# Optimization experiments

Hardware: AMD Instinct MI355X
Metric: run time of the kernel (lower is better)

Reference implementation:

```python
import jax, jax.numpy as jnp
import numpy as np

B, T, D = 2, 2048, 1024
H = 16
HD = D // H          # 64
WIN = 512            # sliding window size


def _band_mask(t, win):
    i = jnp.arange(t)[:, None]
    j = jnp.arange(t)[None, :]
    return ((j <= i) & (j > i - win)).astype(jnp.float32)


def setup_inputs() -> dict:
    key = jax.random.key(0)
    ks = jax.random.split(key, 7)
    s = 0.02
    return {
        "x":  jax.random.normal(ks[0], (B, T, D), dtype=jnp.float32),
        "Wg": jax.random.normal(ks[1], (D, D), dtype=jnp.float32) * s,
        "bg": jnp.zeros((D,), dtype=jnp.float32),
        "Wv": jax.random.normal(ks[2], (D, H * HD), dtype=jnp.float32) * s,
        "bv": jnp.zeros((H * HD,), dtype=jnp.float32),
        "Wo": jax.random.normal(ks[3], (D, D), dtype=jnp.float32) * s,
        "bo": jnp.zeros((D,), dtype=jnp.float32),
    }


def genetic_fitness(pop, mask):
    # pop: (B,H,T,D_head); mask: (T,T)
    # gene_means[b,h,i,d] = sum_j mask[i,j]*pop[b,h,j,d] / active_counts[i]
    counts = jnp.maximum(mask.sum(axis=1), 1.0)                 # (T,)
    gene_means = jnp.einsum('ij,bhjd->bhid', mask, pop) / counts[None, None, :, None]
    denom = gene_means + 0.5                                    # (B,H,T,Dh)
    sum_inv = (1.0 / denom).sum(axis=-1, keepdims=True)
    gene_fit = 1.0 / (denom * sum_inv)                          # (B,H,T,Dh)
    # org_fitness[b,h,i,j] = mask[i,j] * <gene_fit[b,h,i], pop[b,h,j]>
    org = mask[None, None] * jnp.einsum('bhid,bhjd->bhij', gene_fit, pop)
    row = jnp.maximum(org.sum(axis=-1, keepdims=True), 1e-10)
    return org / row                                            # (B,H,T,T)


def reference(x, Wg, bg, Wv, bv, Wo, bo):
    mask = _band_mask(T, WIN)
    g = (x @ Wg + bg).reshape(B, T, H, HD).transpose(0, 2, 1, 3)   # (B,H,T,Dh)
    v = (x @ Wv + bv).reshape(B, T, H, HD).transpose(0, 2, 1, 3)   # (B,H,T,Dh)
    attn = genetic_fitness(g, mask)                                 # (B,H,T,T)
    out = jnp.einsum('bhij,bhjd->bhid', attn, v)                    # (B,H,T,Dh)
    out = out.transpose(0, 2, 1, 3).reshape(B, T, D)
    return out @ Wo + bo
```

## Files before the change

### kernel.cpp

```cpp
#include <hip/hip_runtime.h>

#define NB 2
#define NT 2048
#define ND 1024
#define NH 16
#define HD 64
#define WIN 512
#define NBH (NB*NH)
#define NCH (NT/64)

typedef short    bf16x8 __attribute__((ext_vector_type(8)));
typedef unsigned short us8 __attribute__((ext_vector_type(8)));
typedef unsigned short us4 __attribute__((ext_vector_type(4)));
typedef float    f32x4  __attribute__((ext_vector_type(4)));

__device__ __forceinline__ void fma16(const float4 av, const float4 bv, float acc[4][4])
{
    float ar[4] = {av.x, av.y, av.z, av.w};
    float br[4] = {bv.x, bv.y, bv.z, bv.w};
#pragma unroll
    for (int r = 0; r < 4; ++r)
#pragma unroll
        for (int c = 0; c < 4; ++c)
            acc[r][c] = fmaf(ar[r], br[c], acc[r][c]);
}

__device__ __forceinline__ void split_bf16(float f, unsigned short& h, unsigned short& l)
{
    unsigned u = __float_as_uint(f);
    h = (unsigned short)(u >> 16);
    float fh = __uint_as_float(u & 0xffff0000u);
    l = (unsigned short)(__float_as_uint(f - fh) >> 16);
}

__device__ __forceinline__ unsigned short bf_rne(float f)
{
    unsigned u = __float_as_uint(f);
    u += 0x7fffu + ((u >> 16) & 1u);
    return (unsigned short)(u >> 16);
}

__device__ __forceinline__ us8 pack8(float4 a, float4 b)
{
    us8 r;
    r[0] = bf_rne(a.x); r[1] = bf_rne(a.y); r[2] = bf_rne(a.z); r[3] = bf_rne(a.w);
    r[4] = bf_rne(b.x); r[5] = bf_rne(b.y); r[6] = bf_rne(b.z); r[7] = bf_rne(b.w);
    return r;
}

__global__ __launch_bounds__(256)
void gemm_k(const float* __restrict__ A, const float* __restrict__ W,
            const float* __restrict__ bias, float* __restrict__ C,
            int M, int N, int K)
{
    __shared__ float As[16][64];
    __shared__ float Bs[16][64];
    const int tid = threadIdx.x;
    const int tx = tid & 15, ty = tid >> 4;
    const int n0 = blockIdx.x << 6, m0 = blockIdx.y << 6;
    const int am = tid >> 2, ak = (tid & 3) << 2;
    const int bk = tid >> 4, bn = (tid & 15) << 2;
    const float* Ap = A + (size_t)(m0 + am) * K + ak;
    const float* Wp = W + (size_t)bk * N + n0 + bn;

    float4 a4 = *(const float4*)(Ap);
    float4 b4 = *(const float4*)(Wp);
    float acc[4][4] = {};
    for (int k0 = 0; k0 < K; k0 += 16) {
        __syncthreads();
        {
            const int sw = (tid & 3) << 4;
            As[ak + 0][am ^ sw] = a4.x;
            As[ak + 1][am ^ sw] = a4.y;
            As[ak + 2][am ^ sw] = a4.z;
            As[ak + 3][am ^ sw] = a4.w;
            *(float4*)&Bs[bk][bn] = b4;
        }
        __syncthreads();
        if (k0 + 16 < K) {
            a4 = *(const float4*)(Ap + k0 + 16);
            b4 = *(const float4*)(Wp + (size_t)(k0 + 16) * N);
        }
#pragma unroll
        for (int k = 0; k < 16; ++k) {
            const float4 av = *(const float4*)&As[k][(ty << 2) ^ ((k & 12) << 2)];
            const float4 bv = *(const float4*)&Bs[k][tx << 2];
            fma16(av, bv, acc);
        }
    }
    const float4 bias4 = *(const float4*)&bias[n0 + (tx << 2)];
    const float bb[4] = {bias4.x, bias4.y, bias4.z, bias4.w};
#pragma unroll
    for (int r = 0; r < 4; ++r) {
        const int row = m0 + (ty << 2) + r;
        float4 o;
        o.x = acc[r][0] + bb[0]; o.y = acc[r][1] + bb[1];
        o.z = acc[r][2] + bb[2]; o.w = acc[r][3] + bb[3];
        const int b = row >> 11;
        const int i = row & (NT - 1);
        const int h = n0 >> 6;
        *(float4*)&C[((((size_t)(b * NH + h)) << 11) + i) * HD + (tx << 2)] = o;
    }
}

template<int MODE>
__global__ __launch_bounds__(256)
void mgemm_k(const unsigned short* __restrict__ Ahi, const unsigned short* __restrict__ Alo,
             const unsigned short* __restrict__ Bhi, const unsigned short* __restrict__ Blo,
             const float* __restrict__ bias, float* __restrict__ C,
             int M, int N, int K)
{
    __shared__ unsigned short As[2][128 * 32];
    __shared__ unsigned short Bs[2][128 * 32];
    const int tid = threadIdx.x;
    const int wave = tid >> 6, lane = tid & 63;
    const int wm = wave >> 1, wn = wave & 1;
    const int m0 = blockIdx.y << 7, n0 = blockIdx.x << 7;

    const int srow = tid >> 1, skh = tid & 1;
    const int ssw = (srow & 3) ^ ((srow >> 2) & 3);
    const int sA0 = srow * 32 + ((((skh << 1) | 0) ^ ssw) << 3);
    const int sA1 = srow * 32 + ((((skh << 1) | 1) ^ ssw) << 3);
    const size_t aoff = (size_t)(m0 + srow) * K + (skh << 4);
    const size_t boff = (size_t)(n0 + srow) * K + (skh << 4);

    us8 ah0 = *(const us8*)(Ahi + aoff), ah1 = *(const us8*)(Ahi + aoff + 8);
    us8 al0 = *(const us8*)(Alo + aoff), al1 = *(const us8*)(Alo + aoff + 8);
    us8 bh0 = *(const us8*)(Bhi + boff), bh1 = *(const us8*)(Bhi + boff + 8);
    us8 bl0 = *(const us8*)(Blo + boff), bl1 = *(const us8*)(Blo + boff + 8);

    const int fsw = ((lane >> 4) ^ (lane & 3) ^ ((lane & 12) >> 2)) << 3;

    f32x4 acc[4][4] = {};
    for (int k0 = 0; k0 < K; k0 += 32) {
        __syncthreads();
        *(us8*)&As[0][sA0] = ah0; *(us8*)&As[0][sA1] = ah1;
        *(us8*)&As[1][sA0] = al0; *(us8*)&As[1][sA1] = al1;
        *(us8*)&Bs[0][sA0] = bh0; *(us8*)&Bs[0][sA1] = bh1;
        *(us8*)&Bs[1][sA0] = bl0; *(us8*)&Bs[1][sA1] = bl1;
        __syncthreads();
        if (k0 + 32 < K) {
            const size_t ka = aoff + k0 + 32, kb = boff + k0 + 32;
            ah0 = *(const us8*)(Ahi + ka); ah1 = *(const us8*)(Ahi + ka + 8);
            al0 = *(const us8*)(Alo + ka); al1 = *(const us8*)(Alo + ka + 8);
            bh0 = *(const us8*)(Bhi + kb); bh1 = *(const us8*)(Bhi + kb + 8);
            bl0 = *(const us8*)(Blo + kb); bl1 = *(const us8*)(Blo + kb + 8);
        }
        bf16x8 aH[4], aL[4], bH[4], bL[4];
#pragma unroll
        for (int s = 0; s < 4; ++s) {
            const int ra = (wm << 6) + (s << 4) + (lane & 15);
            const int rb = (wn << 6) + (s << 4) + (lane & 15);
            aH[s] = *(const bf16x8*)&As[0][ra * 32 + fsw];
            aL[s] = *(const bf16x8*)&As[1][ra * 32 + fsw];
            bH[s] = *(const bf16x8*)&Bs[0][rb * 32 + fsw];
            bL[s] = *(const bf16x8*)&Bs[1][rb * 32 + fsw];
        }
#pragma unroll
        for (int ms = 0; ms < 4; ++ms)
#pragma unroll
            for (int ns = 0; ns < 4; ++ns) {
                acc[ms][ns] = __builtin_amdgcn_mfma_f32_16x16x32_bf16(aH[ms], bH[ns], acc[ms][ns], 0, 0, 0);
                acc[ms][ns] = __builtin_amdgcn_mfma_f32_16x16x32_bf16(aH[ms], bL[ns], acc[ms][ns], 0, 0, 0);
                acc[ms][ns] = __builtin_amdgcn_mfma_f32_16x16x32_bf16(aL[ms], bH[ns], acc[ms][ns], 0, 0, 0);
            }
    }

#pragma unroll
    for (int ms = 0; ms < 4; ++ms)
#pragma unroll
        for (int ns = 0; ns < 4; ++ns) {
            const int col = n0 + (wn << 6) + (ns << 4) + (lane & 15);
            const float bb = bias[col];
#pragma unroll
            for (int r = 0; r < 4; ++r) {
                const int row = m0 + (wm << 6) + (ms << 4) + ((lane >> 4) << 2) + r;
                const float val = acc[ms][ns][r] + bb;
                if (MODE == 0) {
                    C[(size_t)row * N + col] = val;
                } else {
                    const int b = row >> 11, i = row & (NT - 1);
                    const int h = col >> 6;
                    C[((((size_t)(b * NH + h)) << 11) + i) * HD + (col & 63)] = val;
                }
            }
        }
}

__global__ __launch_bounds__(256)
void split_k(const float* __restrict__ x, unsigned short* __restrict__ xh,
             unsigned short* __restrict__ xl)
{
    const int e0 = (blockIdx.x * 256 + threadIdx.x) << 2;
    const float4 v = *(const float4*)&x[e0];
    ushort4 hh, ll;
    split_bf16(v.x, hh.x, ll.x); split_bf16(v.y, hh.y, ll.y);
    split_bf16(v.z, hh.z, ll.z); split_bf16(v.w, hh.w, ll.w);
    *(ushort4*)&xh[e0] = hh;
    *(ushort4*)&xl[e0] = ll;
}

__global__ __launch_bounds__(256)
void tsplit_k(const float* __restrict__ W, unsigned short* __restrict__ Th,
              unsigned short* __restrict__ Tl)
{
    __shared__ float Ls[64][68];
    const int n0 = blockIdx.x << 6, k0 = blockIdx.y << 6;
    const int tid = threadIdx.x;
    const int r16 = tid >> 4, c4 = (tid & 15) << 2;
#pragma unroll
    for (int j = 0; j < 4; ++j) {
        const int row = r16 + (j << 4);
        *(float4*)&Ls[row][c4] = *(const float4*)&W[(size_t)(k0 + row) * ND + n0 + c4];
    }
    __syncthreads();
#pragma unroll
    for (int j = 0; j < 4; ++j) {
        const int n = r16 + (j << 4);
        ushort4 hh, ll;
        split_bf16(Ls[c4 + 0][n], hh.x, ll.x);
        split_bf16(Ls[c4 + 1][n], hh.y, ll.y);
        split_bf16(Ls[c4 + 2][n], hh.z, ll.z);
        split_bf16(Ls[c4 + 3][n], hh.w, ll.w);
        const size_t o = (size_t)(n0 + n) * ND + k0 + c4;
        *(ushort4*)&Th[o] = hh;
        *(ushort4*)&Tl[o] = ll;
    }
}

__global__ __launch_bounds__(64)
void chunkscan_k(const float* __restrict__ g, float* __restrict__ Pin,
                 float* __restrict__ Csum)
{
    const int blk = blockIdx.x;
    const int lane = threadIdx.x;
    const int base = (blk << 12) + lane;
    float run = 0.f;
#pragma unroll 16
    for (int t = 0; t < 64; ++t) {
        run += g[base + (t << 6)];
        Pin[base + (t << 6)] = run;
    }
    Csum[(blk << 6) + lane] = run;
}

__global__ __launch_bounds__(64)
void chunkpre_k(const float* __restrict__ Csum, float* __restrict__ Cpre)
{
    const int bh = blockIdx.x, lane = threadIdx.x;
    float run = 0.f;
    for (int c = 0; c < NCH; ++c) {
        run += Csum[((bh * NCH + c) << 6) + lane];
        Cpre[((bh * NCH + c) << 6) + lane] = run;
    }
}

__global__ __launch_bounds__(256)
void winsum_k(const float* __restrict__ Pin, const float* __restrict__ Cpre,
              float* __restrict__ wout)
{
    const int idx = blockIdx.x * 256 + threadIdx.x;
    const int e0 = idx << 2;
    const int row = e0 >> 6;
    const int d = e0 & 63;
    const int bh = row >> 11;
    const int i = row & (NT - 1);
    const int c = i >> 6;

    float4 p = *(const float4*)&Pin[e0];
    float ax = p.x, ay = p.y, az = p.z, aw = p.w;
    if (c > 0) {
        const float4 q = *(const float4*)&Cpre[((bh * NCH + c - 1) << 6) + d];
        ax += q.x; ay += q.y; az += q.z; aw += q.w;
    }
    if (i >= WIN) {
        const int i2 = i - WIN;
        const int c2 = i2 >> 6;
        const float4 p2 = *(const float4*)&Pin[(((bh << 11) + i2) << 6) + d];
        ax -= p2.x; ay -= p2.y; az -= p2.z; aw -= p2.w;
        if (c2 > 0) {
            const float4 q2 = *(const float4*)&Cpre[((bh * NCH + c2 - 1) << 6) + d];
            ax -= q2.x; ay -= q2.y; az -= q2.z; aw -= q2.w;
        }
    }
    *(float4*)&wout[e0] = make_float4(ax, ay, az, aw);
}

__global__ __launch_bounds__(256)
void stats_k(float* __restrict__ wing, double* __restrict__ rowsum)
{
    const int row = (blockIdx.x << 2) + (threadIdx.x >> 6);
    const int lane = threadIdx.x & 63;
    const int i = row & (NT - 1);
    const float w = wing[(row << 6) + lane];
    const double cnt = (double)((i + 1 < WIN) ? (i + 1) : WIN);
    const double denom = (double)w / cnt + 0.5;
    double s = 1.0 / denom;
#pragma unroll
    for (int off = 32; off > 0; off >>= 1) s += __shfl_xor(s, off);
    const double gf = 1.0 / (denom * s);
    double rw = gf * (double)w;
#pragma unroll
    for (int off = 32; off > 0; off >>= 1) rw += __shfl_xor(rw, off);
    wing[(row << 6) + lane] = (float)gf;
    if (lane == 0) rowsum[row] = rw;
}

__global__ __launch_bounds__(256)
void attn_k(const float* __restrict__ gf, const float* __restrict__ g,
            const float* __restrict__ v, const double* __restrict__ rowsum,
            unsigned short* __restrict__ aoh, unsigned short* __restrict__ aol)
{
    __shared__ unsigned short gL[64 * 72];
    __shared__ unsigned short VT[64 * 72];
    __shared__ unsigned short SL[64 * 72];

    const int bh = blockIdx.y, it = blockIdx.x;
    const int i0 = it << 6;
    const int tid = threadIdx.x;
    const int wave = tid >> 6, lane = tid & 63;
    const int l15 = lane & 15, l4 = lane >> 4;

    bf16x8 gfB[2];
    {
        const int ig = i0 + (wave << 4) + l15;
        const float* src = gf + (((size_t)(bh << 11) + ig) << 6) + (l4 << 3);
        const float4 q0 = *(const float4*)(src);
        const float4 q1 = *(const float4*)(src + 4);
        const float4 q2 = *(const float4*)(src + 32);
        const float4 q3 = *(const float4*)(src + 36);
        const us8 f0 = pack8(q0, q1), f1 = pack8(q2, q3);
        gfB[0] = (bf16x8)f0;
        gfB[1] = (bf16x8)f1;
    }

    const int sj = lane, sd0 = wave << 4;

    const int t_lo = (it >= 8) ? (it - 8) : 0;
    float4 gq[4], vq[4];
    {
        const float* gsrc = g + (((size_t)(bh << 11) + (t_lo << 6) + sj) << 6) + sd0;
        const float* vsrc = v + (((size_t)(bh << 11) + (t_lo << 6) + sj) << 6) + sd0;
#pragma unroll
        for (int q = 0; q < 4; ++q) gq[q] = *(const float4*)(gsrc + (q << 2));
#pragma unroll
        for (int q = 0; q < 4; ++q) vq[q] = *(const float4*)(vsrc + (q << 2));
    }

    f32x4 acc2[4] = {};
    const int ig_mask = i0 + (wave << 4) + l15;

    for (int t = t_lo; t <= it; ++t) {
        const int j0 = t << 6;
        __syncthreads();
        {
            *(us8*)&gL[sj * 72 + sd0]     = pack8(gq[0], gq[1]);
            *(us8*)&gL[sj * 72 + sd0 + 8] = pack8(gq[2], gq[3]);
            const float* vf = (const float*)vq;
#pragma unroll
            for (int h = 0; h < 16; ++h)
                VT[(sd0 + h) * 72 + sj] = bf_rne(vf[h]);
        }
        __syncthreads();

        if (t < it) {
            const float* gsrc = g + (((size_t)(bh << 11) + j0 + 64 + sj) << 6) + sd0;
            const float* vsrc = v + (((size_t)(bh << 11) + j0 + 64 + sj) << 6) + sd0;
#pragma unroll
            for (int q = 0; q < 4; ++q) gq[q] = *(const float4*)(gsrc + (q << 2));
#pragma unroll
            for (int q = 0; q < 4; ++q) vq[q] = *(const float4*)(vsrc + (q << 2));
        }

        f32x4 sfr[4] = {};
#pragma unroll
        for (int kk = 0; kk < 2; ++kk)
#pragma unroll
            for (int jm = 0; jm < 4; ++jm) {
                const bf16x8 ag = *(const bf16x8*)&gL[((jm << 4) + l15) * 72 + (kk << 5) + (l4 << 3)];
                sfr[jm] = __builtin_amdgcn_mfma_f32_16x16x32_bf16(ag, gfB[kk], sfr[jm], 0, 0, 0);
            }

        const bool need_mask = (t == it) || (t == it - 8);
#pragma unroll
        for (int jm = 0; jm < 4; ++jm) {
            float s0 = sfr[jm][0], s1 = sfr[jm][1], s2 = sfr[jm][2], s3 = sfr[jm][3];
            if (need_mask) {
                const int jb = j0 + (jm << 4) + (l4 << 2);
                if (!(jb + 0 <= ig_mask && jb + 0 > ig_mask - WIN)) s0 = 0.f;
                if (!(jb + 1 <= ig_mask && jb + 1 > ig_mask - WIN)) s1 = 0.f;
                if (!(jb + 2 <= ig_mask && jb + 2 > ig_mask - WIN)) s2 = 0.f;
                if (!(jb + 3 <= ig_mask && jb + 3 > ig_mask - WIN)) s3 = 0.f;
            }
            us4 sl;
            sl[0] = bf_rne(s0); sl[1] = bf_rne(s1); sl[2] = bf_rne(s2); sl[3] = bf_rne(s3);
            *(us4*)&SL[((wave << 4) + l15) * 72 + (jm << 4) + (l4 << 2)] = sl;
        }

#pragma unroll
        for (int kk = 0; kk < 2; ++kk) {
            const bf16x8 a2 = *(const bf16x8*)&SL[((wave << 4) + l15) * 72 + (kk << 5) + (l4 << 3)];
#pragma unroll
            for (int nf = 0; nf < 4; ++nf) {
                const bf16x8 b2 = *(const bf16x8*)&VT[((nf << 4) + l15) * 72 + (kk << 5) + (l4 << 3)];
                acc2[nf] = __builtin_amdgcn_mfma_f32_16x16x32_bf16(a2, b2, acc2[nf], 0, 0, 0);
            }
        }
    }

    const int b = bh >> 4, hh = bh & 15;
    float inv[4];
#pragma unroll
    for (int r = 0; r < 4; ++r) {
        const int ig = i0 + (wave << 4) + (l4 << 2) + r;
        double rs = rowsum[(bh << 11) + ig];
        if (!(rs > 1e-10)) rs = 1e-10;
        inv[r] = (float)(1.0 / rs);
    }
#pragma unroll
    for (int nf = 0; nf < 4; ++nf)
#pragma unroll
        for (int r = 0; r < 4; ++r) {
            const int ig = i0 + (wave << 4) + (l4 << 2) + r;
            const int d = (nf << 4) + l15;
            const float val = acc2[nf][r] * inv[r];
            unsigned short vh, vl;
            split_bf16(val, vh, vl);
            const size_t base = (((size_t)(b * NT + ig)) << 10) + (hh << 6) + d;
            aoh[base] = vh;
            aol[base] = vl;
        }
}

extern "C" void kernel_launch(void* const* d_in, const int* in_sizes, int n_in,
                              void* d_out, int out_size, void* d_ws, size_t ws_size,
                              hipStream_t stream)
{
    const float* x  = (const float*)d_in[0];
    const float* Wg = (const float*)d_in[1];
    const float* bg = (const float*)d_in[2];
    const float* Wv = (const float*)d_in[3];
    const float* bv = (const float*)d_in[4];
    const float* Wo = (const float*)d_in[5];
    const float* bo = (const float*)d_in[6];
    float* out = (float*)d_out;

    const size_t SZ = (size_t)NB * NH * NT * HD;
    const size_t MW = (size_t)ND * ND;
    const size_t CS = (size_t)NBH * NCH * HD;

    float* gbuf = (float*)d_ws;
    float* vbuf = gbuf + SZ;
    float* pinb = vbuf + SZ;
    float* winb = pinb + SZ;
    float* wpl  = winb + SZ;
    float* csum = wpl + 2 * MW;
    float* cpre = csum + CS;
    double* rsum = (double*)(cpre + CS);

    unsigned short* xhi  = (unsigned short*)winb;
    unsigned short* xlo  = xhi + SZ;
    unsigned short* wvTh = (unsigned short*)wpl;
    unsigned short* wvTl = wvTh + MW;
    unsigned short* woTh = wvTl + MW;
    unsigned short* woTl = woTh + MW;
    unsigned short* aoh  = (unsigned short*)pinb;
    unsigned short* aol  = aoh + SZ;

    const int M = NB * NT;

    gemm_k<<<dim3(ND >> 6, M >> 6), 256, 0, stream>>>(x, Wg, bg, gbuf, M, ND, ND);
    split_k<<<(int)(SZ / 4 / 256), 256, 0, stream>>>(x, xhi, xlo);
    tsplit_k<<<dim3(ND >> 6, ND >> 6), 256, 0, stream>>>(Wv, wvTh, wvTl);
    tsplit_k<<<dim3(ND >> 6, ND >> 6), 256, 0, stream>>>(Wo, woTh, woTl);
    mgemm_k<1><<<dim3(ND >> 7, M >> 7), 256, 0, stream>>>(xhi, xlo, wvTh, wvTl, bv, vbuf, M, ND, ND);
    chunkscan_k<<<NBH * NCH, 64, 0, stream>>>(gbuf, pinb, csum);
    chunkpre_k<<<NBH, 64, 0, stream>>>(csum, cpre);
    winsum_k<<<(NBH * NT * HD / 4) / 256, 256, 0, stream>>>(pinb, cpre, winb);
    stats_k<<<(NBH * NT) / 4, 256, 0, stream>>>(winb, rsum);
    attn_k<<<dim3(NT >> 6, NBH), 256, 0, stream>>>(winb, gbuf, vbuf, rsum, aoh, aol);
    mgemm_k<0><<<dim3(ND >> 7, M >> 7), 256, 0, stream>>>(aoh, aol, woTh, woTl, bo, out, M, ND, ND);
}
```

Before: 388.7 us.

## Compute g projection with three-way bf16-split MFMA GEMM instead of FP32 SIMT

The FP32 SIMT GEMM for the g projection is replaced by a matrix-core GEMM. Both x and Wg are split into three bf16 parts, and six cross products are accumulated to keep near-FP32 accuracy. The goal is to move the largest projection from vector ALUs to MFMA units. The cost is extra split and transpose-split kernels, more workspace, and six times the MFMA work. The split of x now uses round-to-nearest for its high and middle parts, and these are also reused for the v projection.

```diff
diff --git a/kernel.cpp b/kernel.cpp
--- a/kernel.cpp
+++ b/kernel.cpp
@@ -14,17 +14,6 @@
 typedef unsigned short us4 __attribute__((ext_vector_type(4)));
 typedef float    f32x4  __attribute__((ext_vector_type(4)));
 
-__device__ __forceinline__ void fma16(const float4 av, const float4 bv, float acc[4][4])
-{
-    float ar[4] = {av.x, av.y, av.z, av.w};
-    float br[4] = {bv.x, bv.y, bv.z, bv.w};
-#pragma unroll
-    for (int r = 0; r < 4; ++r)
-#pragma unroll
-        for (int c = 0; c < 4; ++c)
-            acc[r][c] = fmaf(ar[r], br[c], acc[r][c]);
-}
-
 __device__ __forceinline__ void split_bf16(float f, unsigned short& h, unsigned short& l)
 {
     unsigned u = __float_as_uint(f);
@@ -40,6 +29,18 @@
     return (unsigned short)(u >> 16);
 }
 
+__device__ __forceinline__ void split3(float f, unsigned short& h,
+                                       unsigned short& m, unsigned short& l)
+{
+    h = bf_rne(f);
+    const float fh = __uint_as_float((unsigned)h << 16);
+    const float r1 = f - fh;
+    m = bf_rne(r1);
+    const float fm = __uint_as_float((unsigned)m << 16);
+    const float r2 = r1 - fm;
+    l = bf_rne(r2);
+}
+
 __device__ __forceinline__ us8 pack8(float4 a, float4 b)
 {
     us8 r;
@@ -49,58 +50,97 @@
 }
 
 __global__ __launch_bounds__(256)
-void gemm_k(const float* __restrict__ A, const float* __restrict__ W,
-            const float* __restrict__ bias, float* __restrict__ C,
-            int M, int N, int K)
-{
-    __shared__ float As[16][64];
-    __shared__ float Bs[16][64];
+void mgemm3_k(const unsigned short* __restrict__ Ah, const unsigned short* __restrict__ Am,
+              const unsigned short* __restrict__ Al,
+              const unsigned short* __restrict__ Bh, const unsigned short* __restrict__ Bm,
+              const unsigned short* __restrict__ Bl,
+              const float* __restrict__ bias, float* __restrict__ C,
+              int M, int N, int K)
+{
+    __shared__ unsigned short As[3][128 * 32];
+    __shared__ unsigned short Bs[3][128 * 32];
     const int tid = threadIdx.x;
-    const int tx = tid & 15, ty = tid >> 4;
-    const int n0 = blockIdx.x << 6, m0 = blockIdx.y << 6;
-    const int am = tid >> 2, ak = (tid & 3) << 2;
-    const int bk = tid >> 4, bn = (tid & 15) << 2;
-    const float* Ap = A + (size_t)(m0 + am) * K + ak;
-    const float* Wp = W + (size_t)bk * N + n0 + bn;
-
-    float4 a4 = *(const float4*)(Ap);
-    float4 b4 = *(const float4*)(Wp);
-    float acc[4][4] = {};
-    for (int k0 = 0; k0 < K; k0 += 16) {
+    const int wave = tid >> 6, lane = tid & 63;
+    const int wm = wave >> 1, wn = wave & 1;
+    const int m0 = blockIdx.y << 7, n0 = blockIdx.x << 7;
+    const int l15 = lane & 15;
+
+    const int srow = tid >> 1, skh = tid & 1;
+    const int ssw = (srow & 3) ^ ((srow >> 2) & 3);
+    const int sA0 = srow * 32 + ((((skh << 1) | 0) ^ ssw) << 3);
+    const int sA1 = srow * 32 + ((((skh << 1) | 1) ^ ssw) << 3);
+    const size_t aoff = (size_t)(m0 + srow) * K + (skh << 4);
+    const size_t boff = (size_t)(n0 + srow) * K + (skh << 4);
+
+    us8 a0[2], a1[2], a2[2], b0[2], b1[2], b2[2];
+    a0[0] = *(const us8*)(Ah + aoff); a0[1] = *(const us8*)(Ah + aoff + 8);
+    a1[0] = *(const us8*)(Am + aoff); a1[1] = *(const us8*)(Am + aoff + 8);
+    a2[0] = *(const us8*)(Al + aoff); a2[1] = *(const us8*)(Al + aoff + 8);
+    b0[0] = *(const us8*)(Bh + boff); b0[1] = *(const us8*)(Bh + boff + 8);
+    b1[0] = *(const us8*)(Bm + boff); b1[1] = *(const us8*)(Bm + boff + 8);
+    b2[0] = *(const us8*)(Bl + boff); b2[1] = *(const us8*)(Bl + boff + 8);
+
+    const int fsw = ((lane >> 4) ^ (lane & 3) ^ ((lane & 12) >> 2)) << 3;
+
+    f32x4 acc[4][4] = {};
+    for (int k0 = 0; k0 < K; k0 += 32) {
         __syncthreads();
-        {
-            const int sw = (tid & 3) << 4;
-            As[ak + 0][am ^ sw] = a4.x;
-            As[ak + 1][am ^ sw] = a4.y;
-            As[ak + 2][am ^ sw] = a4.z;
-            As[ak + 3][am ^ sw] = a4.w;
-            *(float4*)&Bs[bk][bn] = b4;
-        }
+        *(us8*)&As[0][sA0] = a0[0]; *(us8*)&As[0][sA1] = a0[1];
+        *(us8*)&As[1][sA0] = a1[0]; *(us8*)&As[1][sA1] = a1[1];
+        *(us8*)&As[2][sA0] = a2[0]; *(us8*)&As[2][sA1] = a2[1];
+        *(us8*)&Bs[0][sA0] = b0[0]; *(us8*)&Bs[0][sA1] = b0[1];
+        *(us8*)&Bs[1][sA0] = b1[0]; *(us8*)&Bs[1][sA1] = b1[1];
+        *(us8*)&Bs[2][sA0] = b2[0]; *(us8*)&Bs[2][sA1] = b2[1];
         __syncthreads();
-        if (k0 + 16 < K) {
-            a4 = *(const float4*)(Ap + k0 + 16);
-            b4 = *(const float4*)(Wp + (size_t)(k0 + 16) * N);
-        }
-#pragma unroll
-        for (int k = 0; k < 16; ++k) {
-            const float4 av = *(const float4*)&As[k][(ty << 2) ^ ((k & 12) << 2)];
-            const float4 bv = *(const float4*)&Bs[k][tx << 2];
-            fma16(av, bv, acc);
-        }
-    }
-    const float4 bias4 = *(const float4*)&bias[n0 + (tx << 2)];
-    const float bb[4] = {bias4.x, bias4.y, bias4.z, bias4.w};
-#pragma unroll
-    for (int r = 0; r < 4; ++r) {
-        const int row = m0 + (ty << 2) + r;
-        float4 o;
-        o.x = acc[r][0] + bb[0]; o.y = acc[r][1] + bb[1];
-        o.z = acc[r][2] + bb[2]; o.w = acc[r][3] + bb[3];
-        const int b = row >> 11;
-        const int i = row & (NT - 1);
-        const int h = n0 >> 6;
-        *(float4*)&C[((((size_t)(b * NH + h)) << 11) + i) * HD + (tx << 2)] = o;
-    }
+        if (k0 + 32 < K) {
+            const size_t ka = aoff + k0 + 32, kb = boff + k0 + 32;
+            a0[0] = *(const us8*)(Ah + ka); a0[1] = *(const us8*)(Ah + ka + 8);
+            a1[0] = *(const us8*)(Am + ka); a1[1] = *(const us8*)(Am + ka + 8);
+            a2[0] = *(const us8*)(Al + ka); a2[1] = *(const us8*)(Al + ka + 8);
+            b0[0] = *(const us8*)(Bh + kb); b0[1] = *(const us8*)(Bh + kb + 8);
+            b1[0] = *(const us8*)(Bm + kb); b1[1] = *(const us8*)(Bm + kb + 8);
+            b2[0] = *(const us8*)(Bl + kb); b2[1] = *(const us8*)(Bl + kb + 8);
+        }
+        bf16x8 aF[3][4], bF[3][4];
+#pragma unroll
+        for (int s = 0; s < 4; ++s) {
+            const int ra = (wm << 6) + (s << 4) + l15;
+            const int rb = (wn << 6) + (s << 4) + l15;
+#pragma unroll
+            for (int p = 0; p < 3; ++p) {
+                aF[p][s] = *(const bf16x8*)&As[p][ra * 32 + fsw];
+                bF[p][s] = *(const bf16x8*)&Bs[p][rb * 32 + fsw];
+            }
+        }
+#pragma unroll
+        for (int ms = 0; ms < 4; ++ms)
+#pragma unroll
+            for (int ns = 0; ns < 4; ++ns) {
+                f32x4 t = acc[ms][ns];
+                t = __builtin_amdgcn_mfma_f32_16x16x32_bf16(aF[0][ms], bF[0][ns], t, 0, 0, 0);
+                t = __builtin_amdgcn_mfma_f32_16x16x32_bf16(aF[0][ms], bF[1][ns], t, 0, 0, 0);
+                t = __builtin_amdgcn_mfma_f32_16x16x32_bf16(aF[1][ms], bF[0][ns], t, 0, 0, 0);
+                t = __builtin_amdgcn_mfma_f32_16x16x32_bf16(aF[0][ms], bF[2][ns], t, 0, 0, 0);
+                t = __builtin_amdgcn_mfma_f32_16x16x32_bf16(aF[2][ms], bF[0][ns], t, 0, 0, 0);
+                t = __builtin_amdgcn_mfma_f32_16x16x32_bf16(aF[1][ms], bF[1][ns], t, 0, 0, 0);
+                acc[ms][ns] = t;
+            }
+    }
+
+#pragma unroll
+    for (int ms = 0; ms < 4; ++ms)
+#pragma unroll
+        for (int ns = 0; ns < 4; ++ns) {
+            const int col = n0 + (wn << 6) + (ns << 4) + l15;
+            const float bb = bias[col];
+            const int h = col >> 6, d = col & 63;
+#pragma unroll
+            for (int r = 0; r < 4; ++r) {
+                const int row = m0 + (wm << 6) + (ms << 4) + ((lane >> 4) << 2) + r;
+                const int b = row >> 11, i = row & (NT - 1);
+                C[((((size_t)(b * NH + h)) << 11) + i) * HD + d] = acc[ms][ns][r] + bb;
+            }
+        }
 }
 
 template<int MODE>
@@ -188,15 +228,16 @@
 }
 
 __global__ __launch_bounds__(256)
-void split_k(const float* __restrict__ x, unsigned short* __restrict__ xh,
-             unsigned short* __restrict__ xl)
+void split3_k(const float* __restrict__ x, unsigned short* __restrict__ xh,
+              unsigned short* __restrict__ xm, unsigned short* __restrict__ xl)
 {
     const int e0 = (blockIdx.x * 256 + threadIdx.x) << 2;
     const float4 v = *(const float4*)&x[e0];
-    ushort4 hh, ll;
-    split_bf16(v.x, hh.x, ll.x); split_bf16(v.y, hh.y, ll.y);
-    split_bf16(v.z, hh.z, ll.z); split_bf16(v.w, hh.w, ll.w);
+    ushort4 hh, mm, ll;
+    split3(v.x, hh.x, mm.x, ll.x); split3(v.y, hh.y, mm.y, ll.y);
+    split3(v.z, hh.z, mm.z, ll.z); split3(v.w, hh.w, mm.w, ll.w);
     *(ushort4*)&xh[e0] = hh;
+    *(ushort4*)&xm[e0] = mm;
     *(ushort4*)&xl[e0] = ll;
 }
 
@@ -225,6 +266,35 @@
         const size_t o = (size_t)(n0 + n) * ND + k0 + c4;
         *(ushort4*)&Th[o] = hh;
         *(ushort4*)&Tl[o] = ll;
+    }
+}
+
+__global__ __launch_bounds__(256)
+void tsplit3_k(const float* __restrict__ W, unsigned short* __restrict__ T0,
+               unsigned short* __restrict__ T1, unsigned short* __restrict__ T2)
+{
+    __shared__ float Ls[64][68];
+    const int n0 = blockIdx.x << 6, k0 = blockIdx.y << 6;
+    const int tid = threadIdx.x;
+    const int r16 = tid >> 4, c4 = (tid & 15) << 2;
+#pragma unroll
+    for (int j = 0; j < 4; ++j) {
+        const int row = r16 + (j << 4);
+        *(float4*)&Ls[row][c4] = *(const float4*)&W[(size_t)(k0 + row) * ND + n0 + c4];
+    }
+    __syncthreads();
+#pragma unroll
+    for (int j = 0; j < 4; ++j) {
+        const int n = r16 + (j << 4);
+        ushort4 hh, mm, ll;
+        split3(Ls[c4 + 0][n], hh.x, mm.x, ll.x);
+        split3(Ls[c4 + 1][n], hh.y, mm.y, ll.y);
+        split3(Ls[c4 + 2][n], hh.z, mm.z, ll.z);
+        split3(Ls[c4 + 3][n], hh.w, mm.w, ll.w);
+        const size_t o = (size_t)(n0 + n) * ND + k0 + c4;
+        *(ushort4*)&T0[o] = hh;
+        *(ushort4*)&T1[o] = mm;
+        *(ushort4*)&T2[o] = ll;
     }
 }
 
@@ -454,26 +524,33 @@
     float* pinb = vbuf + SZ;
     float* winb = pinb + SZ;
     float* wpl  = winb + SZ;
-    float* csum = wpl + 2 * MW;
-    float* cpre = csum + CS;
-    double* rsum = (double*)(cpre + CS);
-
-    unsigned short* xhi  = (unsigned short*)winb;
-    unsigned short* xlo  = xhi + SZ;
+
     unsigned short* wvTh = (unsigned short*)wpl;
     unsigned short* wvTl = wvTh + MW;
     unsigned short* woTh = wvTl + MW;
     unsigned short* woTl = woTh + MW;
-    unsigned short* aoh  = (unsigned short*)pinb;
-    unsigned short* aol  = aoh + SZ;
+    unsigned short* wgT0 = woTl + MW;
+    unsigned short* wgT1 = wgT0 + MW;
+    unsigned short* wgT2 = wgT1 + MW;
+
+    float* csum = (float*)wgT0;
+    float* cpre = csum + CS;
+    double* rsum = (double*)(cpre + CS);
+
+    unsigned short* xh  = (unsigned short*)winb;
+    unsigned short* xm  = xh + SZ;
+    unsigned short* xl  = (unsigned short*)pinb;
+    unsigned short* aoh = (unsigned short*)pinb;
+    unsigned short* aol = aoh + SZ;
 
     const int M = NB * NT;
 
-    gemm_k<<<dim3(ND >> 6, M >> 6), 256, 0, stream>>>(x, Wg, bg, gbuf, M, ND, ND);
-    split_k<<<(int)(SZ / 4 / 256), 256, 0, stream>>>(x, xhi, xlo);
+    split3_k<<<(int)(SZ / 4 / 256), 256, 0, stream>>>(x, xh, xm, xl);
+    tsplit3_k<<<dim3(ND >> 6, ND >> 6), 256, 0, stream>>>(Wg, wgT0, wgT1, wgT2);
     tsplit_k<<<dim3(ND >> 6, ND >> 6), 256, 0, stream>>>(Wv, wvTh, wvTl);
     tsplit_k<<<dim3(ND >> 6, ND >> 6), 256, 0, stream>>>(Wo, woTh, woTl);
-    mgemm_k<1><<<dim3(ND >> 7, M >> 7), 256, 0, stream>>>(xhi, xlo, wvTh, wvTl, bv, vbuf, M, ND, ND);
+    mgemm3_k<<<dim3(ND >> 7, M >> 7), 256, 0, stream>>>(xh, xm, xl, wgT0, wgT1, wgT2, bg, gbuf, M, ND, ND);
+    mgemm_k<1><<<dim3(ND >> 7, M >> 7), 256, 0, stream>>>(xh, xm, wvTh, wvTl, bv, vbuf, M, ND, ND);
     chunkscan_k<<<NBH * NCH, 64, 0, stream>>>(gbuf, pinb, csum);
     chunkpre_k<<<NBH, 64, 0, stream>>>(csum, cpre);
     winsum_k<<<(NBH * NT * HD / 4) / 256, 256, 0, stream>>>(pinb, cpre, winb);
```

Measured after the change: 340.7 us. -12.4%, faster.
